# Optimization experiments

Measured on AMD Instinct MI355X. Metric: run time of the kernel, lower is better.

## Reference

```python
import jax, jax.numpy as jnp
import numpy as np

B, Q, S, C, D = 32, 128, 2048, 1024, 1024  # batch, query steps, ctx steps, ctx dim, query dim


def setup_inputs() -> dict:
    key = jax.random.key(0)
    k1, k2, k3, k4 = jax.random.split(key, 4)
    context = jax.random.normal(k1, (B, S, C), jnp.float32)
    query = jax.random.normal(k2, (Q, B, D), jnp.float32)
    context_mask = jax.random.randint(k3, (B, S), 0, 2).astype(bool)  # True = masked out
    weights = jax.random.normal(k4, (C, D), jnp.float32)  # nn.Parameter(...).normal_()
    return {"context": context, "query": query, "context_mask": context_mask, "weights": weights}


def reference(context, query, context_mask, weights):
    # Bilinear scores: (context @ W) bmm query^T -> [B, Q, S]; transposed to [Q, B, S]
    # for the per-query-step scan. temp = 1.0 so no rescaling.
    scores = jnp.einsum('bsc,cd,qbd->qbs', context, weights, query)
    neg_inf = jnp.asarray(-jnp.inf, scores.dtype)

    def step(accum, score):  # accum, score: [B, S]
        adj = jnp.where(context_mask, neg_inf, score - accum)  # coverage-adjusted score
        a = jax.nn.softmax(adj, axis=-1)
        return accum + a, a

    accum0 = jnp.zeros((B, S), scores.dtype)
    accum, attention = jax.lax.scan(step, accum0, scores)  # attention: [Q, B, S]

    # compute_composition=True branch; torch returns attention permuted to [Q, B, S],
    # accum [B, 1, S], composition [Q, B, C].
    composition = jnp.einsum('qbs,bsc->qbc', attention, context)
    return attention, accum[:, None, :], composition
```

## Files before the change

### kernel.cpp

```cpp
#include <hip/hip_runtime.h>

#define B_ 32
#define Q_ 128
#define S_ 2048
#define C_ 1024
#define D_ 1024

typedef __attribute__((ext_vector_type(8))) short bf16x8;
typedef __attribute__((ext_vector_type(4))) float f32x4;
typedef __attribute__((ext_vector_type(4))) unsigned int u32x4;

static __device__ __forceinline__ unsigned short f2bf(float f) {
  unsigned int u = __float_as_uint(f);
  u = (u + 0x7FFFu + ((u >> 16) & 1u)) >> 16;
  return (unsigned short)u;
}
static __device__ __forceinline__ float bf2f(unsigned short h) {
  return __uint_as_float(((unsigned int)h) << 16);
}

static __device__ __forceinline__ void gl_lds16(const void* g, void* l) {
  __builtin_amdgcn_global_load_lds(
      (const __attribute__((address_space(1))) unsigned int*)g,
      (__attribute__((address_space(3))) unsigned int*)l, 16, 0, 0);
}

template <int CTRL>
static __device__ __forceinline__ float dpp_ror(float v) {
  return __uint_as_float((unsigned int)__builtin_amdgcn_update_dpp(
      0, (int)__float_as_uint(v), CTRL, 0xf, 0xf, false));
}

static __device__ __forceinline__ void split8(const f32x4 x0, const f32x4 x1,
                                              bf16x8& hi, bf16x8& lo) {
  u32x4 h, l;
#pragma unroll
  for (int p = 0; p < 2; ++p) {
    const unsigned int a0 = __float_as_uint(x0[2 * p]);
    const unsigned int a1 = __float_as_uint(x0[2 * p + 1]);
    h[p] = __builtin_amdgcn_perm(a1, a0, 0x07060302u);
    const float r0 = x0[2 * p]     - __uint_as_float(a0 & 0xffff0000u);
    const float r1 = x0[2 * p + 1] - __uint_as_float(a1 & 0xffff0000u);
    l[p] = __builtin_amdgcn_perm(__float_as_uint(r1), __float_as_uint(r0), 0x07060302u);
  }
#pragma unroll
  for (int p = 0; p < 2; ++p) {
    const unsigned int a0 = __float_as_uint(x1[2 * p]);
    const unsigned int a1 = __float_as_uint(x1[2 * p + 1]);
    h[2 + p] = __builtin_amdgcn_perm(a1, a0, 0x07060302u);
    const float r0 = x1[2 * p]     - __uint_as_float(a0 & 0xffff0000u);
    const float r1 = x1[2 * p + 1] - __uint_as_float(a1 & 0xffff0000u);
    l[2 + p] = __builtin_amdgcn_perm(__float_as_uint(r1), __float_as_uint(r0), 0x07060302u);
  }
  hi = __builtin_bit_cast(bf16x8, h);
  lo = __builtin_bit_cast(bf16x8, l);
}

template <bool FUSE>
__global__ __launch_bounds__(256, 2)
void gemm_f32(const float* __restrict__ Aip, const float* __restrict__ Bip,
              float* __restrict__ outp, int K,
              long aBatch, long bBatch, long outBatch,
              long aRstride, long bRstride, long outRstride, int remapQB,
              unsigned short* __restrict__ fuseOut, long fuseRstride) {
  extern __shared__ char smem[];
  float* sA = (float*)smem;
  float* sB = sA + 8192;

  const int tid = threadIdx.x;
  const int lane = tid & 63;
  const int w = tid >> 6;
  const int wr = w >> 1;
  const int wc = w & 1;
  const int m0 = blockIdx.y * 128;
  const int n0 = blockIdx.x * 128;
  const int bz = blockIdx.z;
  const int frow = lane & 15;
  const int cc = lane >> 4;

  const float* Af = Aip + (long)bz * aBatch;
  const float* Bf = Bip + (long)bz * bBatch;

  f32x4 acc[4][4];
#pragma unroll
  for (int i = 0; i < 4; ++i)
#pragma unroll
    for (int j = 0; j < 4; ++j) acc[i][j] = (f32x4){0.f, 0.f, 0.f, 0.f};

  auto STAGE = [&](int ktt, int bufi) {
#pragma unroll
    for (int i = 0; i < 4; ++i) {
      const int rr = (w * 4 + i) * 8 + (lane >> 3);
      const int cs = (lane & 7) ^ (rr & 7);
      gl_lds16(Af + (long)(m0 + rr) * aRstride + ktt + cs * 4,
               sA + bufi * 4096 + (w * 4 + i) * 256);
    }
#pragma unroll
    for (int i = 0; i < 4; ++i) {
      const int rr = (w * 4 + i) * 8 + (lane >> 3);
      const int cs = (lane & 7) ^ (rr & 7);
      gl_lds16(Bf + (long)(n0 + rr) * bRstride + ktt + cs * 4,
               sB + bufi * 4096 + (w * 4 + i) * 256);
    }
  };

  const int nt = K >> 5;
  STAGE(0, 0);
  STAGE(32, 1);

  for (int t = 0; t < nt; ++t) {
    if (t + 1 < nt) { asm volatile("s_waitcnt vmcnt(8)" ::: "memory"); }
    else            { asm volatile("s_waitcnt vmcnt(0)" ::: "memory"); }
    __builtin_amdgcn_sched_barrier(0);
    asm volatile("s_barrier" ::: "memory");

    const float* sAb = sA + (t & 1) * 4096;
    const float* sBb = sB + (t & 1) * 4096;

    bf16x8 ah[4], al[4], bh[4], bl[4];
#pragma unroll
    for (int i = 0; i < 4; ++i) {
      const int row = wr * 64 + i * 16 + frow;
      const int c0 = ((cc * 2) ^ (row & 7)) << 2;
      const int c1 = ((cc * 2 + 1) ^ (row & 7)) << 2;
      split8(*(const f32x4*)(sAb + row * 32 + c0),
             *(const f32x4*)(sAb + row * 32 + c1), ah[i], al[i]);
    }
#pragma unroll
    for (int j = 0; j < 4; ++j) {
      const int row = wc * 64 + j * 16 + frow;
      const int c0 = ((cc * 2) ^ (row & 7)) << 2;
      const int c1 = ((cc * 2 + 1) ^ (row & 7)) << 2;
      split8(*(const f32x4*)(sBb + row * 32 + c0),
             *(const f32x4*)(sBb + row * 32 + c1), bh[j], bl[j]);
    }
#pragma unroll
    for (int i = 0; i < 4; ++i)
#pragma unroll
      for (int j = 0; j < 4; ++j) {
        acc[i][j] = __builtin_amdgcn_mfma_f32_16x16x32_bf16(ah[i], bh[j], acc[i][j], 0, 0, 0);
        acc[i][j] = __builtin_amdgcn_mfma_f32_16x16x32_bf16(ah[i], bl[j], acc[i][j], 0, 0, 0);
        acc[i][j] = __builtin_amdgcn_mfma_f32_16x16x32_bf16(al[i], bh[j], acc[i][j], 0, 0, 0);
      }

    if constexpr (FUSE) {
      const int k = lane & 31;
      const int nb = w * 32 + ((lane >> 5) << 4);
      unsigned short vals[16];
#pragma unroll
      for (int i = 0; i < 16; ++i) {
        const int row = nb + i;
        vals[i] = f2bf(sBb[row * 32 + (((k >> 2) ^ (row & 7)) << 2) + (k & 3)]);
      }
      unsigned short* dst = fuseOut + ((long)bz * K + t * 32 + k) * fuseRstride + n0 + nb;
      *(bf16x8*)(dst + 0) = *(const bf16x8*)(vals + 0);
      *(bf16x8*)(dst + 8) = *(const bf16x8*)(vals + 8);
    }

    asm volatile("s_barrier" ::: "memory");
    if (t + 2 < nt) STAGE((t + 2) * 32, t & 1);
  }

  float* out = outp + (long)bz * outBatch;
#pragma unroll
  for (int i = 0; i < 4; ++i) {
#pragma unroll
    for (int rr = 0; rr < 4; ++rr) {
      const int grow = m0 + wr * 64 + i * 16 + ((lane >> 4) << 2) + rr;
      const long orow = remapQB ? ((long)(grow & 31) * 128 + (grow >> 5)) : (long)grow;
      float* orp = out + orow * outRstride;
#pragma unroll
      for (int j = 0; j < 4; ++j) {
        const int col = n0 + wc * 64 + j * 16 + (lane & 15);
        orp[col] = acc[i][j][rr];
      }
    }
  }
}

__global__ __launch_bounds__(256, 2)
void gemm_bf16(const unsigned short* __restrict__ Aip, const unsigned short* __restrict__ Bip,
               float* __restrict__ outp, int K,
               long aBatch, long bBatch, long outBatch,
               long aRstride, long bRstride, long outRstride) {
  extern __shared__ char smem[];
  unsigned short* sA = (unsigned short*)smem;
  unsigned short* sB = sA + 16384;

  const int tid = threadIdx.x;
  const int lane = tid & 63;
  const int w = tid >> 6;
  const int wr = w >> 1;
  const int wc = w & 1;
  const int m0 = blockIdx.y * 128;
  const int n0 = blockIdx.x * 128;
  const int bz = blockIdx.z;
  const int frow = lane & 15;
  const int cc = lane >> 4;

  const unsigned short* Ab = Aip + (long)bz * aBatch;
  const unsigned short* Bb = Bip + (long)bz * bBatch;

  f32x4 acc[4][4];
#pragma unroll
  for (int i = 0; i < 4; ++i)
#pragma unroll
    for (int j = 0; j < 4; ++j) acc[i][j] = (f32x4){0.f, 0.f, 0.f, 0.f};

  auto STAGE = [&](int ktt, int bufi) {
#pragma unroll
    for (int i = 0; i < 4; ++i) {
      const int rr = (w * 4 + i) * 8 + (lane >> 3);
      const int cs = (lane & 7) ^ (rr & 7);
      gl_lds16(Ab + (long)(m0 + rr) * aRstride + ktt + cs * 8,
               sA + bufi * 8192 + (w * 4 + i) * 512);
    }
#pragma unroll
    for (int i = 0; i < 4; ++i) {
      const int rr = (w * 4 + i) * 8 + (lane >> 3);
      const int cs = (lane & 7) ^ (rr & 7);
      gl_lds16(Bb + (long)(n0 + rr) * bRstride + ktt + cs * 8,
               sB + bufi * 8192 + (w * 4 + i) * 512);
    }
  };

  const int nt = K >> 6;
  STAGE(0, 0);
  STAGE(64, 1);

  for (int t = 0; t < nt; ++t) {
    if (t + 1 < nt) { asm volatile("s_waitcnt vmcnt(8)" ::: "memory"); }
    else            { asm volatile("s_waitcnt vmcnt(0)" ::: "memory"); }
    __builtin_amdgcn_sched_barrier(0);
    asm volatile("s_barrier" ::: "memory");

    const unsigned short* sAb = sA + (t & 1) * 8192;
    const unsigned short* sBb = sB + (t & 1) * 8192;

#pragma unroll
    for (int kk = 0; kk < 2; ++kk) {
      bf16x8 ah[4], bh[4];
#pragma unroll
      for (int i = 0; i < 4; ++i) {
        const int row = wr * 64 + i * 16 + frow;
        const int ch = kk * 4 + cc;
        ah[i] = *(const bf16x8*)((const char*)sAb + row * 128 + ((ch ^ (row & 7)) << 4));
      }
#pragma unroll
      for (int j = 0; j < 4; ++j) {
        const int row = wc * 64 + j * 16 + frow;
        const int ch = kk * 4 + cc;
        bh[j] = *(const bf16x8*)((const char*)sBb + row * 128 + ((ch ^ (row & 7)) << 4));
      }
#pragma unroll
      for (int i = 0; i < 4; ++i)
#pragma unroll
        for (int j = 0; j < 4; ++j)
          acc[i][j] = __builtin_amdgcn_mfma_f32_16x16x32_bf16(ah[i], bh[j], acc[i][j], 0, 0, 0);
    }

    asm volatile("s_barrier" ::: "memory");
    if (t + 2 < nt) STAGE((t + 2) * 64, t & 1);
  }

  float* out = outp + (long)bz * outBatch;
#pragma unroll
  for (int i = 0; i < 4; ++i) {
#pragma unroll
    for (int rr = 0; rr < 4; ++rr) {
      const int grow = m0 + wr * 64 + i * 16 + ((lane >> 4) << 2) + rr;
      float* orp = out + (long)grow * outRstride;
#pragma unroll
      for (int j = 0; j < 4; ++j) {
        const int col = n0 + wc * 64 + j * 16 + (lane & 15);
        orp[col] = acc[i][j][rr];
      }
    }
  }
}

template <int VMA, int VMB>
static __device__ __forceinline__ void scan_row(
    float* __restrict__ attn, unsigned short* __restrict__ attnb,
    int b, int q, int lane, int wid, int s0,
    const bool* msk, float* acc, f32x4& buf, const f32x4& bufNext,
    float& Mprov, float2 (&red)[2][8]) {
  const float L2E = 1.4426950408889634f;

  if constexpr (VMA == 1)      asm volatile("s_waitcnt vmcnt(1)" ::: "memory");
  else if constexpr (VMA == 3) asm volatile("s_waitcnt vmcnt(3)" ::: "memory");
  else                         asm volatile("s_waitcnt vmcnt(5)" ::: "memory");
  __builtin_amdgcn_sched_barrier(0);

  float adj[4];
#pragma unroll
  for (int j = 0; j < 4; ++j)
    adj[j] = msk[j] ? -1e30f : (buf[j] - acc[j]);

  int pr = q + 2; if (pr > Q_ - 1) pr = Q_ - 1;
  const float* pp = attn + ((long)(pr * B_ + b)) * S_ + s0;
  asm volatile("global_load_dwordx4 %0, %1, off"
               : "=&v"(buf)
               : "v"(pp), "v"(adj[0]), "v"(adj[1]), "v"(adj[2]), "v"(adj[3])
               : "memory");

  float e[4];
#pragma unroll
  for (int j = 0; j < 4; ++j) {
    const float x = exp2f((adj[j] - Mprov) * L2E);
    e[j] = msk[j] ? 0.f : x;
  }

  float ls = (e[0] + e[1]) + (e[2] + e[3]);
  ls += dpp_ror<0x121>(ls);
  ls += dpp_ror<0x122>(ls);
  ls += dpp_ror<0x124>(ls);
  ls += dpp_ror<0x128>(ls);
  ls += __shfl_xor(ls, 16);
  ls += __shfl_xor(ls, 32);

  if constexpr (VMB == 1) asm volatile("s_waitcnt vmcnt(1)" ::: "memory");
  else                    asm volatile("s_waitcnt vmcnt(3)" ::: "memory");
  __builtin_amdgcn_sched_barrier(0);
  float ap[4];
#pragma unroll
  for (int j = 0; j < 4; ++j)
    ap[j] = msk[j] ? -1e30f : (bufNext[j] - acc[j]);
  float lmp = fmaxf(fmaxf(ap[0], ap[1]), fmaxf(ap[2], ap[3]));
  lmp = fmaxf(lmp, dpp_ror<0x121>(lmp));
  lmp = fmaxf(lmp, dpp_ror<0x122>(lmp));
  lmp = fmaxf(lmp, dpp_ror<0x124>(lmp));
  lmp = fmaxf(lmp, dpp_ror<0x128>(lmp));
  lmp = fmaxf(lmp, __shfl_xor(lmp, 16));
  lmp = fmaxf(lmp, __shfl_xor(lmp, 32));

  const int p = q & 1;
  if (lane == 0) red[p][wid] = make_float2(ls, lmp);
  asm volatile("s_waitcnt lgkmcnt(0)\n\ts_barrier" ::: "memory");

  const float2 v0 = red[p][0], v1 = red[p][1], v2 = red[p][2], v3 = red[p][3];
  const float2 v4 = red[p][4], v5 = red[p][5], v6 = red[p][6], v7 = red[p][7];
  const float tot = ((v0.x + v1.x) + (v2.x + v3.x)) + ((v4.x + v5.x) + (v6.x + v7.x));
  const float Mn = fmaxf(fmaxf(fmaxf(v0.y, v1.y), fmaxf(v2.y, v3.y)),
                         fmaxf(fmaxf(v4.y, v5.y), fmaxf(v6.y, v7.y)));
  const float scale = 1.0f / tot;

  f32x4 av;
#pragma unroll
  for (int j = 0; j < 4; ++j) {
    av[j] = e[j] * scale;
    acc[j] += av[j];
  }
  *(f32x4*)(attn + ((long)(q * B_ + b)) * S_ + s0) = av;
  uint2 pk;
  pk.x = (unsigned int)f2bf(av[0]) | ((unsigned int)f2bf(av[1]) << 16);
  pk.y = (unsigned int)f2bf(av[2]) | ((unsigned int)f2bf(av[3]) << 16);
  *(uint2*)(attnb + ((long)b * Q_ + q) * S_ + s0) = pk;

  Mprov = Mn;
}

__global__ __launch_bounds__(512)
void scan_kernel(const int* __restrict__ mask, float* __restrict__ attn,
                 float* __restrict__ accum_out, unsigned short* __restrict__ attnb) {
  const int b = blockIdx.x;
  const int tid = threadIdx.x;
  const int lane = tid & 63;
  const int wid = tid >> 6;
  const int s0 = tid * 4;

  __shared__ float2 red[2][8];

  const int4 mk = *(const int4*)(mask + (long)b * S_ + s0);
  const bool msk[4] = {mk.x != 0, mk.y != 0, mk.z != 0, mk.w != 0};
  asm volatile("" :: "v"(mk.x), "v"(mk.y), "v"(mk.z), "v"(mk.w));

  float acc[4] = {0.f, 0.f, 0.f, 0.f};

  f32x4 bufE, bufO;
  const float* p0 = attn + (long)b * S_ + s0;
  asm volatile("global_load_dwordx4 %0, %1, off" : "=&v"(bufE) : "v"(p0) : "memory");
  const float* p1 = attn + ((long)(B_ + b)) * S_ + s0;
  asm volatile("global_load_dwordx4 %0, %1, off" : "=&v"(bufO) : "v"(p1) : "memory");

  float Mprov;
  {
    asm volatile("s_waitcnt vmcnt(1)" ::: "memory");
    __builtin_amdgcn_sched_barrier(0);
    float a0[4];
#pragma unroll
    for (int j = 0; j < 4; ++j) a0[j] = msk[j] ? -1e30f : bufE[j];
    float lm = fmaxf(fmaxf(a0[0], a0[1]), fmaxf(a0[2], a0[3]));
    lm = fmaxf(lm, dpp_ror<0x121>(lm));
    lm = fmaxf(lm, dpp_ror<0x122>(lm));
    lm = fmaxf(lm, dpp_ror<0x124>(lm));
    lm = fmaxf(lm, dpp_ror<0x128>(lm));
    lm = fmaxf(lm, __shfl_xor(lm, 16));
    lm = fmaxf(lm, __shfl_xor(lm, 32));
    if (lane == 0) red[1][wid] = make_float2(0.f, lm);
    asm volatile("s_waitcnt lgkmcnt(0)\n\ts_barrier" ::: "memory");
    Mprov = red[1][0].y;
#pragma unroll
    for (int w2 = 1; w2 < 8; ++w2) Mprov = fmaxf(Mprov, red[1][w2].y);
  }

  scan_row<1, 1>(attn, attnb, b, 0, lane, wid, s0, msk, acc, bufE, bufO, Mprov, red);
  scan_row<3, 3>(attn, attnb, b, 1, lane, wid, s0, msk, acc, bufO, bufE, Mprov, red);
  for (int q = 2; q < Q_; q += 2) {
    scan_row<5, 3>(attn, attnb, b, q,     lane, wid, s0, msk, acc, bufE, bufO, Mprov, red);
    scan_row<5, 3>(attn, attnb, b, q + 1, lane, wid, s0, msk, acc, bufO, bufE, Mprov, red);
  }

  f32x4 a4;
#pragma unroll
  for (int j = 0; j < 4; ++j) a4[j] = acc[j];
  *(f32x4*)(accum_out + (long)b * S_ + s0) = a4;
}

extern "C" void kernel_launch(void* const* d_in, const int* in_sizes, int n_in,
                              void* d_out, int out_size, void* d_ws, size_t ws_size,
                              hipStream_t stream) {
  const float* ctx   = (const float*)d_in[0];
  const float* query = (const float*)d_in[1];
  const int*   mask  = (const int*)d_in[2];
  const float* W     = (const float*)d_in[3];

  float* out = (float*)d_out;
  float* attn = out;
  float* accum_out = out + (size_t)Q_ * B_ * S_;
  float* comp = accum_out + (size_t)B_ * S_;

  char* ws = (char*)d_ws;
  float* qw = (float*)ws;
  unsigned short* ctxT  = (unsigned short*)(ws + (size_t)16 * 1024 * 1024);
  unsigned short* attnb = (unsigned short*)(ws + (size_t)16 * 1024 * 1024 +
                                            (size_t)B_ * C_ * S_ * 2);

  gemm_f32<false><<<dim3(C_ / 128, (Q_ * B_) / 128, 1), 256, 65536, stream>>>(
      query, W, qw, D_, 0L, 0L, 0L, (long)D_, (long)D_, (long)C_, 1, nullptr, 0L);

  gemm_f32<true><<<dim3(S_ / 128, 1, B_), 256, 65536, stream>>>(
      qw, ctx, attn, C_, (long)Q_ * C_, (long)S_ * C_, (long)S_,
      (long)C_, (long)C_, (long)B_ * S_, 0, ctxT, (long)S_);

  scan_kernel<<<B_, 512, 0, stream>>>(mask, attn, accum_out, attnb);

  gemm_bf16<<<dim3(C_ / 128, 1, B_), 256, 65536, stream>>>(
      attnb, ctxT, comp, S_, (long)Q_ * S_, (long)C_ * S_, (long)C_,
      (long)S_, (long)S_, (long)B_ * C_);
}
```

Before: 286.4 us.

## Drop bf16 attention copy; composition GEMM reads fp32 attention and converts in-kernel

The scan kernel no longer writes a separate bf16 copy of attention in [B,Q,S] layout. The composition GEMM now stages the fp32 attention output directly from the [Q,B,S] buffer into LDS and converts it to bf16 in registers before each MFMA. This cuts the extra write traffic from the latency-bound scan and drops one workspace buffer. In exchange the GEMM moves twice the A-operand bytes, uses 96KB of LDS at occupancy 1, and spends extra VALU work on conversion.

```diff
diff --git a/kernel.cpp b/kernel.cpp
--- a/kernel.cpp
+++ b/kernel.cpp
@@ -54,6 +54,15 @@
   }
   hi = __builtin_bit_cast(bf16x8, h);
   lo = __builtin_bit_cast(bf16x8, l);
+}
+
+static __device__ __forceinline__ bf16x8 cvt8(const f32x4 x0, const f32x4 x1) {
+  bf16x8 r;
+#pragma unroll
+  for (int e = 0; e < 4; ++e) r[e] = (short)f2bf(x0[e]);
+#pragma unroll
+  for (int e = 0; e < 4; ++e) r[4 + e] = (short)f2bf(x1[e]);
+  return r;
 }
 
 template <bool FUSE>
@@ -178,14 +187,14 @@
   }
 }
 
-__global__ __launch_bounds__(256, 2)
-void gemm_bf16(const unsigned short* __restrict__ Aip, const unsigned short* __restrict__ Bip,
+__global__ __launch_bounds__(256, 1)
+void gemm_comp(const float* __restrict__ Aip, const unsigned short* __restrict__ Bip,
                float* __restrict__ outp, int K,
                long aBatch, long bBatch, long outBatch,
                long aRstride, long bRstride, long outRstride) {
   extern __shared__ char smem[];
-  unsigned short* sA = (unsigned short*)smem;
-  unsigned short* sB = sA + 16384;
+  float* sA = (float*)smem;
+  unsigned short* sB = (unsigned short*)(sA + 16384);
 
   const int tid = threadIdx.x;
   const int lane = tid & 63;
@@ -198,7 +207,7 @@
   const int frow = lane & 15;
   const int cc = lane >> 4;
 
-  const unsigned short* Ab = Aip + (long)bz * aBatch;
+  const float* Af = Aip + (long)bz * aBatch;
   const unsigned short* Bb = Bip + (long)bz * bBatch;
 
   f32x4 acc[4][4];
@@ -209,11 +218,11 @@
 
   auto STAGE = [&](int ktt, int bufi) {
 #pragma unroll
-    for (int i = 0; i < 4; ++i) {
-      const int rr = (w * 4 + i) * 8 + (lane >> 3);
-      const int cs = (lane & 7) ^ (rr & 7);
-      gl_lds16(Ab + (long)(m0 + rr) * aRstride + ktt + cs * 8,
-               sA + bufi * 8192 + (w * 4 + i) * 512);
+    for (int i = 0; i < 8; ++i) {
+      const int rr = (w * 8 + i) * 4 + (lane >> 4);
+      const int cs = (lane & 15) ^ (rr & 7);
+      gl_lds16(Af + (long)(m0 + rr) * aRstride + ktt + cs * 4,
+               sA + bufi * 8192 + (w * 8 + i) * 256);
     }
 #pragma unroll
     for (int i = 0; i < 4; ++i) {
@@ -229,12 +238,12 @@
   STAGE(64, 1);
 
   for (int t = 0; t < nt; ++t) {
-    if (t + 1 < nt) { asm volatile("s_waitcnt vmcnt(8)" ::: "memory"); }
+    if (t + 1 < nt) { asm volatile("s_waitcnt vmcnt(12)" ::: "memory"); }
     else            { asm volatile("s_waitcnt vmcnt(0)" ::: "memory"); }
     __builtin_amdgcn_sched_barrier(0);
     asm volatile("s_barrier" ::: "memory");
 
-    const unsigned short* sAb = sA + (t & 1) * 8192;
+    const float* sAb = sA + (t & 1) * 8192;
     const unsigned short* sBb = sB + (t & 1) * 8192;
 
 #pragma unroll
@@ -243,8 +252,11 @@
 #pragma unroll
       for (int i = 0; i < 4; ++i) {
         const int row = wr * 64 + i * 16 + frow;
-        const int ch = kk * 4 + cc;
-        ah[i] = *(const bf16x8*)((const char*)sAb + row * 128 + ((ch ^ (row & 7)) << 4));
+        const int ch = kk * 8 + cc * 2;
+        const int c0 = (ch ^ (row & 7)) << 2;
+        const int c1 = ((ch + 1) ^ (row & 7)) << 2;
+        ah[i] = cvt8(*(const f32x4*)(sAb + row * 64 + c0),
+                     *(const f32x4*)(sAb + row * 64 + c1));
       }
 #pragma unroll
       for (int j = 0; j < 4; ++j) {
@@ -281,15 +293,15 @@
 
 template <int VMA, int VMB>
 static __device__ __forceinline__ void scan_row(
-    float* __restrict__ attn, unsigned short* __restrict__ attnb,
+    float* __restrict__ attn,
     int b, int q, int lane, int wid, int s0,
     const bool* msk, float* acc, f32x4& buf, const f32x4& bufNext,
     float& Mprov, float2 (&red)[2][8]) {
   const float L2E = 1.4426950408889634f;
 
   if constexpr (VMA == 1)      asm volatile("s_waitcnt vmcnt(1)" ::: "memory");
-  else if constexpr (VMA == 3) asm volatile("s_waitcnt vmcnt(3)" ::: "memory");
-  else                         asm volatile("s_waitcnt vmcnt(5)" ::: "memory");
+  else if constexpr (VMA == 2) asm volatile("s_waitcnt vmcnt(2)" ::: "memory");
+  else                         asm volatile("s_waitcnt vmcnt(3)" ::: "memory");
   __builtin_amdgcn_sched_barrier(0);
 
   float adj[4];
@@ -320,7 +332,7 @@
   ls += __shfl_xor(ls, 32);
 
   if constexpr (VMB == 1) asm volatile("s_waitcnt vmcnt(1)" ::: "memory");
-  else                    asm volatile("s_waitcnt vmcnt(3)" ::: "memory");
+  else                    asm volatile("s_waitcnt vmcnt(2)" ::: "memory");
   __builtin_amdgcn_sched_barrier(0);
   float ap[4];
 #pragma unroll
@@ -352,17 +364,13 @@
     acc[j] += av[j];
   }
   *(f32x4*)(attn + ((long)(q * B_ + b)) * S_ + s0) = av;
-  uint2 pk;
-  pk.x = (unsigned int)f2bf(av[0]) | ((unsigned int)f2bf(av[1]) << 16);
-  pk.y = (unsigned int)f2bf(av[2]) | ((unsigned int)f2bf(av[3]) << 16);
-  *(uint2*)(attnb + ((long)b * Q_ + q) * S_ + s0) = pk;
 
   Mprov = Mn;
 }
 
 __global__ __launch_bounds__(512)
 void scan_kernel(const int* __restrict__ mask, float* __restrict__ attn,
-                 float* __restrict__ accum_out, unsigned short* __restrict__ attnb) {
+                 float* __restrict__ accum_out) {
   const int b = blockIdx.x;
   const int tid = threadIdx.x;
   const int lane = tid & 63;
@@ -404,11 +412,11 @@
     for (int w2 = 1; w2 < 8; ++w2) Mprov = fmaxf(Mprov, red[1][w2].y);
   }
 
-  scan_row<1, 1>(attn, attnb, b, 0, lane, wid, s0, msk, acc, bufE, bufO, Mprov, red);
-  scan_row<3, 3>(attn, attnb, b, 1, lane, wid, s0, msk, acc, bufO, bufE, Mprov, red);
+  scan_row<1, 1>(attn, b, 0, lane, wid, s0, msk, acc, bufE, bufO, Mprov, red);
+  scan_row<2, 2>(attn, b, 1, lane, wid, s0, msk, acc, bufO, bufE, Mprov, red);
   for (int q = 2; q < Q_; q += 2) {
-    scan_row<5, 3>(attn, attnb, b, q,     lane, wid, s0, msk, acc, bufE, bufO, Mprov, red);
-    scan_row<5, 3>(attn, attnb, b, q + 1, lane, wid, s0, msk, acc, bufO, bufE, Mprov, red);
+    scan_row<3, 2>(attn, b, q,     lane, wid, s0, msk, acc, bufE, bufO, Mprov, red);
+    scan_row<3, 2>(attn, b, q + 1, lane, wid, s0, msk, acc, bufO, bufE, Mprov, red);
   }
 
   f32x4 a4;
@@ -433,8 +441,6 @@
   char* ws = (char*)d_ws;
   float* qw = (float*)ws;
   unsigned short* ctxT  = (unsigned short*)(ws + (size_t)16 * 1024 * 1024);
-  unsigned short* attnb = (unsigned short*)(ws + (size_t)16 * 1024 * 1024 +
-                                            (size_t)B_ * C_ * S_ * 2);
 
   gemm_f32<false><<<dim3(C_ / 128, (Q_ * B_) / 128, 1), 256, 65536, stream>>>(
       query, W, qw, D_, 0L, 0L, 0L, (long)D_, (long)D_, (long)C_, 1, nullptr, 0L);
@@ -443,9 +449,9 @@
       qw, ctx, attn, C_, (long)Q_ * C_, (long)S_ * C_, (long)S_,
       (long)C_, (long)C_, (long)B_ * S_, 0, ctxT, (long)S_);
 
-  scan_kernel<<<B_, 512, 0, stream>>>(mask, attn, accum_out, attnb);
-
-  gemm_bf16<<<dim3(C_ / 128, 1, B_), 256, 65536, stream>>>(
-      attnb, ctxT, comp, S_, (long)Q_ * S_, (long)C_ * S_, (long)C_,
-      (long)S_, (long)S_, (long)B_ * C_);
-}
+  scan_kernel<<<B_, 512, 0, stream>>>(mask, attn, accum_out);
+
+  gemm_comp<<<dim3(C_ / 128, 1, B_), 256, 98304, stream>>>(
+      attn, ctxT, comp, S_, (long)S_, (long)C_ * S_, (long)C_,
+      (long)B_ * S_, (long)S_, (long)B_ * C_);
+}
```

After: 292.6 us. 2.2% more time.
